# Kernel tuning notes

Hardware: AMD Instinct MI355X
Metric: run time of the kernel (lower is better)

## Reference

```python
import math
import jax, jax.numpy as jnp
import numpy as np

B, T, D, H = 4, 2048, 1024, 16
HD = D // H


def setup_inputs() -> dict:
    key = jax.random.key(0)
    ks = jax.random.split(key, 5)
    s = 1.0 / math.sqrt(D)  # linear-layer-ish init scale
    x = jax.random.normal(ks[0], (B, T, D), dtype=jnp.float32)
    wq = jax.random.normal(ks[1], (D, D), dtype=jnp.float32) * s
    wk = jax.random.normal(ks[2], (D, D), dtype=jnp.float32) * s
    wv = jax.random.normal(ks[3], (D, D), dtype=jnp.float32) * s
    wo = jax.random.normal(ks[4], (D, D), dtype=jnp.float32) * s
    bq = jnp.zeros((D,), jnp.float32)
    bk = jnp.zeros((D,), jnp.float32)
    bv = jnp.zeros((D,), jnp.float32)
    bo = jnp.zeros((D,), jnp.float32)
    # causal 0/1 mask, broadcast over batch and heads: [1, 1, T, T]
    mask = jnp.tril(jnp.ones((T, T), jnp.int32))[None, None]
    return {"x": x, "wq": wq, "bq": bq, "wk": wk, "bk": bk,
            "wv": wv, "bv": bv, "wo": wo, "bo": bo, "mask": mask}


def reference(x, wq, bq, wk, bk, wv, bv, wo, bo, mask):
    b, t, d = x.shape
    # separate QKV linears (x_cond defaults to x -> self-attention)
    q = x @ wq.T + bq
    k = x @ wk.T + bk
    v = x @ wv.T + bv
    # [b, t, h, hd] -> [b, h, t, hd]
    q = q.reshape(b, t, H, HD).transpose(0, 2, 1, 3)
    k = k.reshape(b, t, H, HD).transpose(0, 2, 1, 3)
    v = v.reshape(b, t, H, HD).transpose(0, 2, 1, 3)
    scale = 1.0 / math.sqrt(HD)
    attn = jnp.einsum('bhtd,bhsd->bhts', q, k) * scale  # [b, h, t, t]
    attn = jnp.where(mask[:, :, :t, :t] == 0, jnp.float32(-jnp.inf), attn)
    attn = jax.nn.softmax(attn, axis=-1)
    # dropout is identity in eval mode
    out = jnp.einsum('bhts,bhsd->bhtd', attn, v)  # [b, h, t, hd]
    out = out.transpose(0, 2, 1, 3).reshape(b, t, d)
    return out @ wo.T + bo
```

## Files before the change

kernel.cpp:

```cpp
#include <hip/hip_runtime.h>
#include <cstdint>

typedef __bf16 bf16x8 __attribute__((ext_vector_type(8)));
typedef float f32x4 __attribute__((ext_vector_type(4)));
typedef uint32_t u32x4 __attribute__((ext_vector_type(4)));
typedef unsigned short u16;

#define B_ 4
#define T_ 2048
#define D_ 1024
#define H_ 16
#define HD_ 64
#define M_ (B_*T_)
#define QSCALE 0.1803368801111204f

__device__ __forceinline__ u16 f2bf(float f) {
  union { float f; uint32_t u; } x; x.f = f;
  uint32_t u = x.u;
  uint32_t r = (u + 0x7FFFu + ((u >> 16) & 1u)) >> 16;
  return (u16)r;
}

__device__ __forceinline__ uint32_t pkbf(float a, float b) {
  union { float f; uint32_t u; } x, y; x.f = a; y.f = b;
  uint32_t t0 = x.u + 0x8000u, t1 = y.u + 0x8000u;
  return __builtin_amdgcn_perm(t1, t0, 0x07060302u);
}

__device__ __forceinline__ bf16x8 ld8(const u16* p) {
  return *(const bf16x8*)p;
}

__device__ __forceinline__ void gl_lds16(const u16* g, u16* l) {
  __builtin_amdgcn_global_load_lds(
      (__attribute__((address_space(1))) void*)(g),
      (__attribute__((address_space(3))) void*)(l), 16, 0, 0);
}

__global__ void cvt_all(const float* __restrict__ x, const float* __restrict__ wq,
                        const float* __restrict__ wk, const float* __restrict__ wv,
                        const float* __restrict__ wo,
                        u16* __restrict__ xb, u16* __restrict__ wqb, u16* __restrict__ wkb,
                        u16* __restrict__ wvb, u16* __restrict__ wob) {
  const long NX = (long)M_ * D_;
  long i = ((long)blockIdx.x * 256 + threadIdx.x) * 4;
  const float* s; u16* d; long j;
  if (i < NX) { s = x; d = xb; j = i; }
  else {
    long r = i - NX; int seg = (int)(r >> 20); j = r & ((1 << 20) - 1);
    s = seg == 0 ? wq : seg == 1 ? wk : seg == 2 ? wv : wo;
    d = seg == 0 ? wqb : seg == 1 ? wkb : seg == 2 ? wvb : wob;
  }
  float4 v = *(const float4*)(s + j);
  ushort4 o;
  o.x = f2bf(v.x); o.y = f2bf(v.y); o.z = f2bf(v.z); o.w = f2bf(v.w);
  *(ushort4*)(d + j) = o;
}


template <int PR>
__device__ __forceinline__ void lda_t(bf16x8 (&af)[4][2], const u16* base,
                                      int wr, int lanem, int quad) {
#pragma unroll
  for (int mi = 0; mi < 4; ++mi)
#pragma unroll
    for (int ks = 0; ks < 2; ++ks) {
      int row = wr * 128 + PR * 64 + mi * 16 + lanem;
      int off = row * 128 + ((ks * 64 + quad * 16) ^ ((lanem & 7) << 4));
      af[mi][ks] = ld8((const u16*)((const char*)base + off));
    }
}

template <int PC>
__device__ __forceinline__ void ldb_t(bf16x8 (&bf)[2][2][2], const u16* base,
                                      int wc, int lanem, int quad) {
#pragma unroll
  for (int nj = 0; nj < 2; ++nj)
#pragma unroll
    for (int ks = 0; ks < 2; ++ks) {
      int row = wc * 64 + PC * 32 + nj * 16 + lanem;
      int off = row * 128 + ((ks * 64 + quad * 16) ^ ((lanem & 7) << 4));
      bf[PC][nj][ks] = ld8((const u16*)((const char*)base + off));
    }
}

template <int PR, int PC>
__device__ __forceinline__ void mfma16(f32x4 (&acc)[8][4], const bf16x8 (&af)[4][2],
                                       const bf16x8 (&bf)[2][2][2]) {
#pragma unroll
  for (int mi = 0; mi < 4; ++mi)
#pragma unroll
    for (int nj = 0; nj < 2; ++nj)
#pragma unroll
      for (int ks = 0; ks < 2; ++ks)
        acc[PR * 4 + mi][PC * 2 + nj] = __builtin_amdgcn_mfma_f32_16x16x32_bf16(
            af[mi][ks], bf[PC][nj][ks], acc[PR * 4 + mi][PC * 2 + nj], 0, 0, 0);
}

#define PH_PRE()                                        \
  __builtin_amdgcn_s_barrier();                         \
  asm volatile("s_waitcnt lgkmcnt(0)" ::: "memory");    \
  __builtin_amdgcn_sched_barrier(0);                    \
  __builtin_amdgcn_s_setprio(1)

#define PH_POST()                                       \
  __builtin_amdgcn_s_setprio(0);                        \
  __builtin_amdgcn_s_barrier()

__global__ __launch_bounds__(512, 2)
void gemm_qkv(const u16* __restrict__ A, const u16* __restrict__ Bw,
              const float* __restrict__ bq, const float* __restrict__ bk,
              const float* __restrict__ bv,
              u16* __restrict__ qb, u16* __restrict__ kb, u16* __restrict__ vtb) {
  __shared__ union {
    struct { u16 A[2][256][64]; u16 B[2][256][64]; } t;
    u16 C[128 * 264];
  } sm;

  const int tid = threadIdx.x;
  const int wv = tid >> 6, lane = tid & 63;
  const int lanem = lane & 15, quad = lane >> 4;
  const int wr = wv >> 2, wc = wv & 3;
  const int n0 = blockIdx.x * 256, m0 = blockIdx.y * 256;

  const int grow = lane >> 3;
  const int gcol = (((lane & 7) ^ grow) * 8);

  auto stageA = [&](int buf, int row0, int k0) {
    gl_lds16(A + (size_t)(m0 + row0 + wv * 8 + grow) * D_ + k0 + gcol,
             &sm.t.A[buf][row0 + wv * 8][0]);
  };
  auto stageB = [&](int buf, int row0, int k0) {
    gl_lds16(Bw + (size_t)(n0 + row0 + wv * 8 + grow) * D_ + k0 + gcol,
             &sm.t.B[buf][row0 + wv * 8][0]);
  };

  f32x4 acc[8][4];
#pragma unroll
  for (int a = 0; a < 8; ++a)
#pragma unroll
    for (int b = 0; b < 4; ++b) acc[a][b] = (f32x4){0.f, 0.f, 0.f, 0.f};

  bf16x8 af[4][2];
  bf16x8 bf[2][2][2];

  stageA(0, 0, 0);   stageA(0, 128, 0);
  stageB(0, 0, 0);   stageB(0, 64, 0);
  stageB(0, 128, 0); stageB(0, 192, 0);
  stageA(0, 64, 0);  stageA(0, 192, 0);
  stageA(1, 0, 64);   stageA(1, 128, 64);
  stageB(1, 0, 64);   stageB(1, 64, 64);
  stageB(1, 128, 64); stageB(1, 192, 64);
  asm volatile("s_waitcnt vmcnt(6)" ::: "memory");
  __builtin_amdgcn_s_barrier();

#pragma unroll 2
  for (int kt = 0; kt < 16; ++kt) {
    const int buf = kt & 1;
    const u16* Ab = &sm.t.A[buf][0][0];
    const u16* Bb = &sm.t.B[buf][0][0];
    const int k1 = (kt + 1) << 6, k2 = (kt + 2) << 6;

    lda_t<0>(af, Ab, wr, lanem, quad);
    ldb_t<0>(bf, Bb, wc, lanem, quad);
    if (kt < 15) { stageA(buf ^ 1, 64, k1); stageA(buf ^ 1, 192, k1); }
    PH_PRE();
    mfma16<0, 0>(acc, af, bf);
    PH_POST();

    ldb_t<1>(bf, Bb, wc, lanem, quad);
    if (kt < 14) { stageA(buf, 0, k2); stageA(buf, 128, k2); }
    PH_PRE();
    mfma16<0, 1>(acc, af, bf);
    PH_POST();

    lda_t<1>(af, Ab, wr, lanem, quad);
    if (kt < 14) { stageB(buf, 0, k2); stageB(buf, 64, k2); }
    PH_PRE();
    mfma16<1, 0>(acc, af, bf);
    PH_POST();

    if (kt < 14) { stageB(buf, 128, k2); stageB(buf, 192, k2); }
    __builtin_amdgcn_s_barrier();
    __builtin_amdgcn_s_setprio(1);
    mfma16<1, 1>(acc, af, bf);
    __builtin_amdgcn_s_setprio(0);
    if (kt < 14)       asm volatile("s_waitcnt vmcnt(6)" ::: "memory");
    else if (kt == 14) asm volatile("s_waitcnt vmcnt(0)" ::: "memory");
    __builtin_amdgcn_s_barrier();
  }

  const int seg = n0 >> 10, n0l = n0 & 1023;
  const int bb = m0 >> 11, tl0 = m0 & (T_ - 1);

  if (seg == 2) {
#pragma unroll
    for (int p = 0; p < 2; ++p) {
      __syncthreads();
      if ((wc >> 1) == p) {
#pragma unroll
        for (int pr = 0; pr < 2; ++pr)
#pragma unroll
          for (int mi = 0; mi < 4; ++mi)
#pragma unroll
            for (int pc = 0; pc < 2; ++pc)
#pragma unroll
              for (int nj = 0; nj < 2; ++nj) {
                int nloc = (wc & 1) * 64 + (pc * 2 + nj) * 16 + lanem;
                float bvv = bv[n0l + p * 128 + nloc];
                int mb = wr * 128 + pr * 64 + mi * 16 + quad * 4;
                ushort4 w4;
                w4.x = f2bf(acc[pr * 4 + mi][pc * 2 + nj][0] + bvv);
                w4.y = f2bf(acc[pr * 4 + mi][pc * 2 + nj][1] + bvv);
                w4.z = f2bf(acc[pr * 4 + mi][pc * 2 + nj][2] + bvv);
                w4.w = f2bf(acc[pr * 4 + mi][pc * 2 + nj][3] + bvv);
                *(ushort4*)&sm.C[nloc * 264 + mb] = w4;
              }
      }
      __syncthreads();
#pragma unroll
      for (int it = 0; it < 8; ++it) {
        int chunk = it * 512 + tid;
        int nrow = chunk >> 5, c8 = chunk & 31;
        int gnl = n0l + p * 128 + nrow;
        int hh = gnl >> 6, hd = gnl & 63;
        *(uint4*)&vtb[(((size_t)bb * H_ + hh) * HD_ + hd) * T_ + tl0 + c8 * 8] =
            *(const uint4*)&sm.C[nrow * 264 + c8 * 8];
      }
    }
  } else {
    const float* bias = seg == 0 ? bq : bk;
    u16* out = seg == 0 ? qb : kb;
    const float sc = seg == 0 ? QSCALE : 1.0f;
#pragma unroll
    for (int p = 0; p < 2; ++p) {
      __syncthreads();
      if (wr == p) {
#pragma unroll
        for (int pr = 0; pr < 2; ++pr)
#pragma unroll
          for (int mi = 0; mi < 4; ++mi)
#pragma unroll
            for (int pc = 0; pc < 2; ++pc)
#pragma unroll
              for (int nj = 0; nj < 2; ++nj) {
                int ncol = wc * 64 + (pc * 2 + nj) * 16 + lanem;
                float bvv = bias[n0l + ncol];
                int mrow = pr * 64 + mi * 16 + quad * 4;
#pragma unroll
                for (int i = 0; i < 4; ++i)
                  sm.C[(mrow + i) * 264 + ncol] =
                      f2bf((acc[pr * 4 + mi][pc * 2 + nj][i] + bvv) * sc);
              }
      }
      __syncthreads();
#pragma unroll
      for (int it = 0; it < 8; ++it) {
        int chunk = it * 512 + tid;
        int row = chunk >> 5, c8 = chunk & 31;
        int gc = n0l + c8 * 8;
        int hh = gc >> 6, hd = gc & 63;
        int t = tl0 + p * 128 + row;
        *(uint4*)&out[(((size_t)bb * H_ + hh) * T_ + t) * HD_ + hd] =
            *(const uint4*)&sm.C[row * 264 + c8 * 8];
      }
    }
  }
}

__global__ __launch_bounds__(256, 3)
void gemm_wo(const u16* __restrict__ A, const u16* __restrict__ Bw,
             const float* __restrict__ bias, float* __restrict__ Co) {
  __shared__ u16 S[2][2][4096];
  int tid = threadIdx.x;
  int n0 = blockIdx.x * 128, m0 = blockIdx.y * 128;
  int wv = tid >> 6, lane = tid & 63, lanem = lane & 15, quad = lane >> 4;
  int wm = (wv >> 1) * 64, wn = (wv & 1) * 64;

  int rA = wv * 16 + (lane >> 2);
  int cc = (lane & 3) * 8;
  const u16* Ab = A + (size_t)(m0 + rA) * D_ + cc;
  const u16* Bb = Bw + (size_t)(n0 + rA) * D_ + cc;

  f32x4 acc[4][4];
#pragma unroll
  for (int mi = 0; mi < 4; ++mi)
#pragma unroll
    for (int ni = 0; ni < 4; ++ni)
      acc[mi][ni] = (f32x4){0.f, 0.f, 0.f, 0.f};

  for (int kt = 0; kt < 16; ++kt) {
    int k0 = kt * 64;
    __syncthreads();
#pragma unroll
    for (int ks = 0; ks < 2; ++ks)
#pragma unroll
      for (int j = 0; j < 2; ++j) {
        gl_lds16(Ab + k0 + ks * 32 + (size_t)j * 64 * D_,
                 &S[0][ks][(j * 256 + wv * 64) * 8]);
        gl_lds16(Bb + k0 + ks * 32 + (size_t)j * 64 * D_,
                 &S[1][ks][(j * 256 + wv * 64) * 8]);
      }
    __syncthreads();
#pragma unroll
    for (int ks = 0; ks < 2; ++ks) {
      bf16x8 af[4], bfr[4];
#pragma unroll
      for (int mi = 0; mi < 4; ++mi)
        af[mi] = ld8(&S[0][ks][(wm + mi * 16 + lanem) * 32 + quad * 8]);
#pragma unroll
      for (int ni = 0; ni < 4; ++ni)
        bfr[ni] = ld8(&S[1][ks][(wn + ni * 16 + lanem) * 32 + quad * 8]);
#pragma unroll
      for (int mi = 0; mi < 4; ++mi)
#pragma unroll
        for (int ni = 0; ni < 4; ++ni)
          acc[mi][ni] = __builtin_amdgcn_mfma_f32_16x16x32_bf16(af[mi], bfr[ni], acc[mi][ni], 0, 0, 0);
    }
  }

#pragma unroll
  for (int ni = 0; ni < 4; ++ni) {
    int gn = n0 + wn + ni * 16 + lanem;
    float bvv = bias[gn];
#pragma unroll
    for (int mi = 0; mi < 4; ++mi)
#pragma unroll
      for (int i = 0; i < 4; ++i) {
        int gm = m0 + wm + mi * 16 + quad * 4 + i;
        Co[(size_t)gm * D_ + gn] = acc[mi][ni][i] + bvv;
      }
  }
}

__global__ __launch_bounds__(256, 4)
void flash4(const u16* __restrict__ qb, const u16* __restrict__ kb,
            const u16* __restrict__ vtb, u16* __restrict__ ob) {
  __shared__ u16 Ks[2][2][64][32];
  __shared__ u16 Vs[2][2][64][32];
  int tid = threadIdx.x, wv = tid >> 6, lane = tid & 63;
  int lanem = lane & 15, quad = lane >> 4;
  int h = blockIdx.y, b = blockIdx.z;
  int z = (int)blockIdx.z;
  int qt = ((int)blockIdx.x ^ ((z & 1) * 15) ^ ((z >> 1) * 3)) & 15;
  size_t bh = (size_t)b * H_ + h;
  int qrow0 = qt * 128 + wv * 32;
  const u16* Qg = qb + (bh * T_ + qrow0) * HD_;
  const u16* Kg = kb + bh * T_ * HD_;
  const u16* Vg = vtb + bh * HD_ * T_;

  int slot = tid >> 2, r = slot & 15;
  int key = (slot >> 5) * 32 + (r >> 2) * 8 + ((slot >> 4) & 1) * 4 + (r & 3);
  const u16* gK = Kg + (size_t)key * HD_ + (tid & 3) * 8;
  const u16* gV = Vg + (size_t)slot * T_ + (tid & 3) * 8;

  bf16x8 bq[2][2];
#pragma unroll
  for (int mi = 0; mi < 2; ++mi)
#pragma unroll
    for (int ks = 0; ks < 2; ++ks)
      bq[mi][ks] = ld8(&Qg[(size_t)(mi * 16 + lanem) * HD_ + ks * 32 + quad * 8]);

  f32x4 acc_o[2][4];
  float lsum[2][4];
#pragma unroll
  for (int mi = 0; mi < 2; ++mi) {
#pragma unroll
    for (int c = 0; c < 4; ++c) lsum[mi][c] = 0.f;
#pragma unroll
    for (int ni = 0; ni < 4; ++ni) acc_o[mi][ni] = (f32x4){0.f, 0.f, 0.f, 0.f};
  }

  int nIter = qt * 2 + 2;
  int myTiles = (qrow0 >> 6) + 1;

#define STAGE_KV(bufi, s0c)                                                 \
  do {                                                                      \
    gl_lds16(gK + (size_t)(s0c) * HD_,      &Ks[bufi][0][0][0] + wv * 512); \
    gl_lds16(gK + (size_t)(s0c) * HD_ + 32, &Ks[bufi][1][0][0] + wv * 512); \
    gl_lds16(gV + (s0c),                    &Vs[bufi][0][0][0] + wv * 512); \
    gl_lds16(gV + (s0c) + 32,               &Vs[bufi][1][0][0] + wv * 512); \
  } while (0)

  STAGE_KV(0, 0);
  for (int it = 0; it < nIter; ++it) {
    __builtin_amdgcn_s_waitcnt(0);
    __syncthreads();
    if (it + 1 < nIter) STAGE_KV((it + 1) & 1, (it + 1) * 64);
    if (it >= myTiles) continue;
    int s0 = it * 64, buf = it & 1;

    f32x4 accs[2][4];
#pragma unroll
    for (int mi = 0; mi < 2; ++mi)
#pragma unroll
      for (int ni = 0; ni < 4; ++ni) accs[mi][ni] = (f32x4){0.f, 0.f, 0.f, 0.f};
#pragma unroll
    for (int ks = 0; ks < 2; ++ks)
#pragma unroll
      for (int ni = 0; ni < 4; ++ni) {
        bf16x8 kf = ld8(&Ks[buf][ks][ni * 16 + lanem][quad * 8]);
        accs[0][ni] = __builtin_amdgcn_mfma_f32_16x16x32_bf16(kf, bq[0][ks], accs[0][ni], 0, 0, 0);
        accs[1][ni] = __builtin_amdgcn_mfma_f32_16x16x32_bf16(kf, bq[1][ks], accs[1][ni], 0, 0, 0);
      }

    if (s0 + 63 > qrow0) {
#pragma unroll
      for (int mi = 0; mi < 2; ++mi) {
        int qg = qrow0 + mi * 16 + lanem;
#pragma unroll
        for (int ni = 0; ni < 4; ++ni)
#pragma unroll
          for (int i = 0; i < 4; ++i) {
            int sl = (ni >> 1) * 32 + quad * 8 + (ni & 1) * 4 + i;
            float p = (s0 + sl > qg) ? 0.f : __builtin_amdgcn_exp2f(accs[mi][ni][i]);
            accs[mi][ni][i] = p;
            lsum[mi][i] += p;
          }
      }
    } else {
#pragma unroll
      for (int mi = 0; mi < 2; ++mi)
#pragma unroll
        for (int ni = 0; ni < 4; ++ni)
#pragma unroll
          for (int i = 0; i < 4; ++i) {
            float p = __builtin_amdgcn_exp2f(accs[mi][ni][i]);
            accs[mi][ni][i] = p;
            lsum[mi][i] += p;
          }
    }

#pragma unroll
    for (int c = 0; c < 2; ++c) {
      u32x4 pk0, pk1;
      pk0[0] = pkbf(accs[0][c * 2][0], accs[0][c * 2][1]);
      pk0[1] = pkbf(accs[0][c * 2][2], accs[0][c * 2][3]);
      pk0[2] = pkbf(accs[0][c * 2 + 1][0], accs[0][c * 2 + 1][1]);
      pk0[3] = pkbf(accs[0][c * 2 + 1][2], accs[0][c * 2 + 1][3]);
      pk1[0] = pkbf(accs[1][c * 2][0], accs[1][c * 2][1]);
      pk1[1] = pkbf(accs[1][c * 2][2], accs[1][c * 2][3]);
      pk1[2] = pkbf(accs[1][c * 2 + 1][0], accs[1][c * 2 + 1][1]);
      pk1[3] = pkbf(accs[1][c * 2 + 1][2], accs[1][c * 2 + 1][3]);
      bf16x8 bp0 = __builtin_bit_cast(bf16x8, pk0);
      bf16x8 bp1 = __builtin_bit_cast(bf16x8, pk1);
#pragma unroll
      for (int ni = 0; ni < 4; ++ni) {
        bf16x8 vf = ld8(&Vs[buf][c][ni * 16 + lanem][quad * 8]);
        acc_o[0][ni] = __builtin_amdgcn_mfma_f32_16x16x32_bf16(vf, bp0, acc_o[0][ni], 0, 0, 0);
        acc_o[1][ni] = __builtin_amdgcn_mfma_f32_16x16x32_bf16(vf, bp1, acc_o[1][ni], 0, 0, 0);
      }
    }
  }
#undef STAGE_KV

#pragma unroll
  for (int mi = 0; mi < 2; ++mi) {
    float v = (lsum[mi][0] + lsum[mi][1]) + (lsum[mi][2] + lsum[mi][3]);
    v += __shfl_xor(v, 16);
    v += __shfl_xor(v, 32);
    float inv = 1.f / v;
    int q = qrow0 + mi * 16 + lanem;
    u16* og = ob + ((size_t)b * T_ + q) * D_ + h * HD_;
#pragma unroll
    for (int ni = 0; ni < 4; ++ni) {
      ushort4 st;
      st.x = f2bf(acc_o[mi][ni][0] * inv);
      st.y = f2bf(acc_o[mi][ni][1] * inv);
      st.z = f2bf(acc_o[mi][ni][2] * inv);
      st.w = f2bf(acc_o[mi][ni][3] * inv);
      *(ushort4*)(og + ni * 16 + quad * 4) = st;
    }
  }
}

extern "C" void kernel_launch(void* const* d_in, const int* in_sizes, int n_in,
                              void* d_out, int out_size, void* d_ws, size_t ws_size,
                              hipStream_t stream) {
  const float* x  = (const float*)d_in[0];
  const float* wq = (const float*)d_in[1];
  const float* bq = (const float*)d_in[2];
  const float* wk = (const float*)d_in[3];
  const float* bk = (const float*)d_in[4];
  const float* wv = (const float*)d_in[5];
  const float* bv = (const float*)d_in[6];
  const float* wo = (const float*)d_in[7];
  const float* bo = (const float*)d_in[8];

  char* ws = (char*)d_ws;
  const size_t MB = 1ull << 20;
  u16* xb   = (u16*)(ws + 0 * MB);
  u16* wqkv = (u16*)(ws + 16 * MB);
  u16* wob  = (u16*)(ws + 22 * MB);
  u16* qb   = (u16*)(ws + 24 * MB);
  u16* kb   = (u16*)(ws + 40 * MB);
  u16* vtb  = (u16*)(ws + 56 * MB);
  u16* ob   = (u16*)(ws + 72 * MB);

  cvt_all<<<(M_ * D_ + 4 * D_ * D_) / 1024, 256, 0, stream>>>(
      x, wq, wk, wv, wo, xb, wqkv, wqkv + (size_t)D_ * D_, wqkv + 2 * (size_t)D_ * D_, wob);

  gemm_qkv<<<dim3(3 * D_ / 256, M_ / 256), 512, 0, stream>>>(
      xb, wqkv, bq, bk, bv, qb, kb, vtb);

  flash4<<<dim3(T_ / 128, H_, B_), 256, 0, stream>>>(qb, kb, vtb, ob);

  gemm_wo<<<dim3(D_ / 128, M_ / 128), 256, 0, stream>>>(ob, wob, bo, (float*)d_out);
}
```

Before: 268.9 us.

## Retile QKV GEMM to 256x128 with triple-buffered LDS and XCD-aware block mapping

Shrinks the QKV projection tile from 256x256 to 256x128 and reorganises the eight waves as a 4x2 grid, each computing a 64x64 sub-tile. It also replaces the double-buffered staging with a three-buffer rotation, cutting the phases per k-step from four to two. Blocks launch on a 1-D grid of 768 with a remap that groups consecutive tiles per XCD stride. The aim is better wave quantisation across CUs, since 768 tiles divide more evenly than 384. It also aims for better L2 locality per XCD and deeper prefetch. The cost is less operand reuse per tile and a large LDS footprint, about 144KB.

```diff
diff --git a/kernel.cpp b/kernel.cpp
--- a/kernel.cpp
+++ b/kernel.cpp
@@ -58,43 +58,42 @@
 }
 
 
-template <int PR>
-__device__ __forceinline__ void lda_t(bf16x8 (&af)[4][2], const u16* base,
-                                      int wr, int lanem, int quad) {
-#pragma unroll
-  for (int mi = 0; mi < 4; ++mi)
+template <int PH>
+__device__ __forceinline__ void ldA_ph(bf16x8 (&af)[2][2], const u16* buf,
+                                       int wr, int lanem, int quad) {
+#pragma unroll
+  for (int mi = 0; mi < 2; ++mi)
 #pragma unroll
     for (int ks = 0; ks < 2; ++ks) {
-      int row = wr * 128 + PR * 64 + mi * 16 + lanem;
-      int off = row * 128 + ((ks * 64 + quad * 16) ^ ((lanem & 7) << 4));
-      af[mi][ks] = ld8((const u16*)((const char*)base + off));
-    }
-}
-
-template <int PC>
-__device__ __forceinline__ void ldb_t(bf16x8 (&bf)[2][2][2], const u16* base,
-                                      int wc, int lanem, int quad) {
-#pragma unroll
-  for (int nj = 0; nj < 2; ++nj)
+      int row = wr * 64 + (PH * 2 + mi) * 16 + lanem;
+      int off = row * 64 + ((ks * 32 + quad * 8) ^ ((lanem & 7) << 3));
+      af[mi][ks] = ld8(buf + off);
+    }
+}
+
+__device__ __forceinline__ void ldB_all(bf16x8 (&bfr)[4][2], const u16* buf,
+                                        int wc, int lanem, int quad) {
+#pragma unroll
+  for (int nj = 0; nj < 4; ++nj)
 #pragma unroll
     for (int ks = 0; ks < 2; ++ks) {
-      int row = wc * 64 + PC * 32 + nj * 16 + lanem;
-      int off = row * 128 + ((ks * 64 + quad * 16) ^ ((lanem & 7) << 4));
-      bf[PC][nj][ks] = ld8((const u16*)((const char*)base + off));
-    }
-}
-
-template <int PR, int PC>
-__device__ __forceinline__ void mfma16(f32x4 (&acc)[8][4], const bf16x8 (&af)[4][2],
-                                       const bf16x8 (&bf)[2][2][2]) {
-#pragma unroll
-  for (int mi = 0; mi < 4; ++mi)
-#pragma unroll
-    for (int nj = 0; nj < 2; ++nj)
+      int row = 256 + wc * 64 + nj * 16 + lanem;
+      int off = row * 64 + ((ks * 32 + quad * 8) ^ ((lanem & 7) << 3));
+      bfr[nj][ks] = ld8(buf + off);
+    }
+}
+
+template <int PH>
+__device__ __forceinline__ void mfmaPH(f32x4 (&acc)[4][4], const bf16x8 (&af)[2][2],
+                                       const bf16x8 (&bfr)[4][2]) {
+#pragma unroll
+  for (int mi = 0; mi < 2; ++mi)
+#pragma unroll
+    for (int nj = 0; nj < 4; ++nj)
 #pragma unroll
       for (int ks = 0; ks < 2; ++ks)
-        acc[PR * 4 + mi][PC * 2 + nj] = __builtin_amdgcn_mfma_f32_16x16x32_bf16(
-            af[mi][ks], bf[PC][nj][ks], acc[PR * 4 + mi][PC * 2 + nj], 0, 0, 0);
+        acc[PH * 2 + mi][nj] = __builtin_amdgcn_mfma_f32_16x16x32_bf16(
+            af[mi][ks], bfr[nj][ks], acc[PH * 2 + mi][nj], 0, 0, 0);
 }
 
 #define PH_PRE()                                        \
@@ -113,157 +112,128 @@
               const float* __restrict__ bv,
               u16* __restrict__ qb, u16* __restrict__ kb, u16* __restrict__ vtb) {
   __shared__ union {
-    struct { u16 A[2][256][64]; u16 B[2][256][64]; } t;
-    u16 C[128 * 264];
+    u16 S[3][384][64];
+    u16 C[256 * 136];
   } sm;
 
   const int tid = threadIdx.x;
   const int wv = tid >> 6, lane = tid & 63;
   const int lanem = lane & 15, quad = lane >> 4;
-  const int wr = wv >> 2, wc = wv & 3;
-  const int n0 = blockIdx.x * 256, m0 = blockIdx.y * 256;
+  const int wr = wv >> 1, wc = wv & 1;
+
+  const int l = ((int)blockIdx.x & 7) * 96 + ((int)blockIdx.x >> 3);
+  const int n0 = (l % 24) * 128, m0 = (l / 24) * 256;
 
   const int grow = lane >> 3;
   const int gcol = (((lane & 7) ^ grow) * 8);
 
-  auto stageA = [&](int buf, int row0, int k0) {
-    gl_lds16(A + (size_t)(m0 + row0 + wv * 8 + grow) * D_ + k0 + gcol,
-             &sm.t.A[buf][row0 + wv * 8][0]);
+  auto stage = [&](u16* bufbase, int u, int k0) {
+    const u16* src = (u < 4)
+        ? A  + (size_t)(m0 + u * 64 + wv * 8 + grow) * D_ + k0 + gcol
+        : Bw + (size_t)(n0 + (u - 4) * 64 + wv * 8 + grow) * D_ + k0 + gcol;
+    gl_lds16(src, bufbase + (u * 64 + wv * 8) * 64);
   };
-  auto stageB = [&](int buf, int row0, int k0) {
-    gl_lds16(Bw + (size_t)(n0 + row0 + wv * 8 + grow) * D_ + k0 + gcol,
-             &sm.t.B[buf][row0 + wv * 8][0]);
-  };
-
-  f32x4 acc[8][4];
-#pragma unroll
-  for (int a = 0; a < 8; ++a)
+
+  f32x4 acc[4][4];
+#pragma unroll
+  for (int a = 0; a < 4; ++a)
 #pragma unroll
     for (int b = 0; b < 4; ++b) acc[a][b] = (f32x4){0.f, 0.f, 0.f, 0.f};
 
-  bf16x8 af[4][2];
-  bf16x8 bf[2][2][2];
-
-  stageA(0, 0, 0);   stageA(0, 128, 0);
-  stageB(0, 0, 0);   stageB(0, 64, 0);
-  stageB(0, 128, 0); stageB(0, 192, 0);
-  stageA(0, 64, 0);  stageA(0, 192, 0);
-  stageA(1, 0, 64);   stageA(1, 128, 64);
-  stageB(1, 0, 64);   stageB(1, 64, 64);
-  stageB(1, 128, 64); stageB(1, 192, 64);
+  bf16x8 af[2][2];
+  bf16x8 bfr[4][2];
+
+  u16* p0 = &sm.S[0][0][0];
+  u16* p1 = &sm.S[1][0][0];
+  u16* p2 = &sm.S[2][0][0];
+
+#pragma unroll
+  for (int u = 0; u < 6; ++u) stage(p0, u, 0);
+#pragma unroll
+  for (int u = 0; u < 6; ++u) stage(p1, u, 64);
   asm volatile("s_waitcnt vmcnt(6)" ::: "memory");
   __builtin_amdgcn_s_barrier();
 
-#pragma unroll 2
   for (int kt = 0; kt < 16; ++kt) {
-    const int buf = kt & 1;
-    const u16* Ab = &sm.t.A[buf][0][0];
-    const u16* Bb = &sm.t.B[buf][0][0];
-    const int k1 = (kt + 1) << 6, k2 = (kt + 2) << 6;
-
-    lda_t<0>(af, Ab, wr, lanem, quad);
-    ldb_t<0>(bf, Bb, wc, lanem, quad);
-    if (kt < 15) { stageA(buf ^ 1, 64, k1); stageA(buf ^ 1, 192, k1); }
+    const int k2 = (kt + 2) << 6;
+
+    ldA_ph<0>(af, p0, wr, lanem, quad);
+    ldB_all(bfr, p0, wc, lanem, quad);
+    if (kt < 14) { stage(p2, 0, k2); stage(p2, 1, k2); stage(p2, 2, k2); }
     PH_PRE();
-    mfma16<0, 0>(acc, af, bf);
+    mfmaPH<0>(acc, af, bfr);
     PH_POST();
 
-    ldb_t<1>(bf, Bb, wc, lanem, quad);
-    if (kt < 14) { stageA(buf, 0, k2); stageA(buf, 128, k2); }
-    PH_PRE();
-    mfma16<0, 1>(acc, af, bf);
-    PH_POST();
-
-    lda_t<1>(af, Ab, wr, lanem, quad);
-    if (kt < 14) { stageB(buf, 0, k2); stageB(buf, 64, k2); }
-    PH_PRE();
-    mfma16<1, 0>(acc, af, bf);
-    PH_POST();
-
-    if (kt < 14) { stageB(buf, 128, k2); stageB(buf, 192, k2); }
+    ldA_ph<1>(af, p0, wr, lanem, quad);
+    if (kt < 14) { stage(p2, 3, k2); stage(p2, 4, k2); stage(p2, 5, k2); }
     __builtin_amdgcn_s_barrier();
+    asm volatile("s_waitcnt lgkmcnt(0)" ::: "memory");
+    __builtin_amdgcn_sched_barrier(0);
     __builtin_amdgcn_s_setprio(1);
-    mfma16<1, 1>(acc, af, bf);
+    mfmaPH<1>(acc, af, bfr);
     __builtin_amdgcn_s_setprio(0);
     if (kt < 14)       asm volatile("s_waitcnt vmcnt(6)" ::: "memory");
     else if (kt == 14) asm volatile("s_waitcnt vmcnt(0)" ::: "memory");
     __builtin_amdgcn_s_barrier();
+
+    u16* t = p0; p0 = p1; p1 = p2; p2 = t;
   }
 
   const int seg = n0 >> 10, n0l = n0 & 1023;
   const int bb = m0 >> 11, tl0 = m0 & (T_ - 1);
 
   if (seg == 2) {
-#pragma unroll
-    for (int p = 0; p < 2; ++p) {
-      __syncthreads();
-      if ((wc >> 1) == p) {
-#pragma unroll
-        for (int pr = 0; pr < 2; ++pr)
-#pragma unroll
-          for (int mi = 0; mi < 4; ++mi)
-#pragma unroll
-            for (int pc = 0; pc < 2; ++pc)
-#pragma unroll
-              for (int nj = 0; nj < 2; ++nj) {
-                int nloc = (wc & 1) * 64 + (pc * 2 + nj) * 16 + lanem;
-                float bvv = bv[n0l + p * 128 + nloc];
-                int mb = wr * 128 + pr * 64 + mi * 16 + quad * 4;
-                ushort4 w4;
-                w4.x = f2bf(acc[pr * 4 + mi][pc * 2 + nj][0] + bvv);
-                w4.y = f2bf(acc[pr * 4 + mi][pc * 2 + nj][1] + bvv);
-                w4.z = f2bf(acc[pr * 4 + mi][pc * 2 + nj][2] + bvv);
-                w4.w = f2bf(acc[pr * 4 + mi][pc * 2 + nj][3] + bvv);
-                *(ushort4*)&sm.C[nloc * 264 + mb] = w4;
-              }
-      }
-      __syncthreads();
-#pragma unroll
-      for (int it = 0; it < 8; ++it) {
-        int chunk = it * 512 + tid;
-        int nrow = chunk >> 5, c8 = chunk & 31;
-        int gnl = n0l + p * 128 + nrow;
-        int hh = gnl >> 6, hd = gnl & 63;
-        *(uint4*)&vtb[(((size_t)bb * H_ + hh) * HD_ + hd) * T_ + tl0 + c8 * 8] =
-            *(const uint4*)&sm.C[nrow * 264 + c8 * 8];
-      }
+    __syncthreads();
+#pragma unroll
+    for (int a = 0; a < 4; ++a)
+#pragma unroll
+      for (int nj = 0; nj < 4; ++nj) {
+        int ncol = wc * 64 + nj * 16 + lanem;
+        float bvv = bv[n0l + ncol];
+        int mb = wr * 64 + a * 16 + quad * 4;
+        ushort4 w4;
+        w4.x = f2bf(acc[a][nj][0] + bvv);
+        w4.y = f2bf(acc[a][nj][1] + bvv);
+        w4.z = f2bf(acc[a][nj][2] + bvv);
+        w4.w = f2bf(acc[a][nj][3] + bvv);
+        *(ushort4*)&sm.C[ncol * 264 + mb] = w4;
+      }
+    __syncthreads();
+#pragma unroll
+    for (int it = 0; it < 8; ++it) {
+      int chunk = it * 512 + tid;
+      int nrow = chunk >> 5, c8 = chunk & 31;
+      int gnl = n0l + nrow;
+      int hh = gnl >> 6, hd = gnl & 63;
+      *(uint4*)&vtb[(((size_t)bb * H_ + hh) * HD_ + hd) * T_ + tl0 + c8 * 8] =
+          *(const uint4*)&sm.C[nrow * 264 + c8 * 8];
     }
   } else {
     const float* bias = seg == 0 ? bq : bk;
     u16* out = seg == 0 ? qb : kb;
     const float sc = seg == 0 ? QSCALE : 1.0f;
-#pragma unroll
-    for (int p = 0; p < 2; ++p) {
-      __syncthreads();
-      if (wr == p) {
-#pragma unroll
-        for (int pr = 0; pr < 2; ++pr)
-#pragma unroll
-          for (int mi = 0; mi < 4; ++mi)
-#pragma unroll
-            for (int pc = 0; pc < 2; ++pc)
-#pragma unroll
-              for (int nj = 0; nj < 2; ++nj) {
-                int ncol = wc * 64 + (pc * 2 + nj) * 16 + lanem;
-                float bvv = bias[n0l + ncol];
-                int mrow = pr * 64 + mi * 16 + quad * 4;
-#pragma unroll
-                for (int i = 0; i < 4; ++i)
-                  sm.C[(mrow + i) * 264 + ncol] =
-                      f2bf((acc[pr * 4 + mi][pc * 2 + nj][i] + bvv) * sc);
-              }
-      }
-      __syncthreads();
-#pragma unroll
-      for (int it = 0; it < 8; ++it) {
-        int chunk = it * 512 + tid;
-        int row = chunk >> 5, c8 = chunk & 31;
-        int gc = n0l + c8 * 8;
-        int hh = gc >> 6, hd = gc & 63;
-        int t = tl0 + p * 128 + row;
-        *(uint4*)&out[(((size_t)bb * H_ + hh) * T_ + t) * HD_ + hd] =
-            *(const uint4*)&sm.C[row * 264 + c8 * 8];
-      }
+    __syncthreads();
+#pragma unroll
+    for (int a = 0; a < 4; ++a)
+#pragma unroll
+      for (int nj = 0; nj < 4; ++nj) {
+        int col = wc * 64 + nj * 16 + lanem;
+        float bvv = bias[n0l + col];
+        int r = wr * 64 + a * 16 + quad * 4;
+#pragma unroll
+        for (int i = 0; i < 4; ++i)
+          sm.C[(r + i) * 136 + col] = f2bf((acc[a][nj][i] + bvv) * sc);
+      }
+    __syncthreads();
+#pragma unroll
+    for (int it = 0; it < 8; ++it) {
+      int chunk = it * 512 + tid;
+      int row = chunk >> 4, c8 = chunk & 15;
+      int col0 = c8 * 8;
+      int hh = (n0l + col0) >> 6, hd = col0 & 63;
+      int t = tl0 + row;
+      *(uint4*)&out[(((size_t)bb * H_ + hh) * T_ + t) * HD_ + hd] =
+          *(const uint4*)&sm.C[row * 136 + col0];
     }
   }
 }
@@ -500,8 +470,7 @@
   cvt_all<<<(M_ * D_ + 4 * D_ * D_) / 1024, 256, 0, stream>>>(
       x, wq, wk, wv, wo, xb, wqkv, wqkv + (size_t)D_ * D_, wqkv + 2 * (size_t)D_ * D_, wob);
 
-  gemm_qkv<<<dim3(3 * D_ / 256, M_ / 256), 512, 0, stream>>>(
-      xb, wqkv, bq, bk, bv, qb, kb, vtb);
+  gemm_qkv<<<768, 512, 0, stream>>>(xb, wqkv, bq, bk, bv, qb, kb, vtb);
 
   flash4<<<dim3(T_ / 128, H_, B_), 256, 0, stream>>>(qb, kb, vtb, ob);
 
```

Measured after the change: 269.5 us. No clear change (+0.3%).
